# Kernel optimization log

Measured on AMD Instinct MI355X. Metric: run time of the kernel, lower is better.

The kernel has to match this reference:

```python
import jax, jax.numpy as jnp
import numpy as np

NEG_SLOPE = 0.2  # PyG GATConv default


def _gat_conv(x, src, dst, W, a_src, a_dst, b, heads, out_ch, concat, n):
    """PyG-style GATConv. src/dst already include self-loops. a_*: (heads, out_ch)."""
    h = (x @ W).reshape(n, heads, out_ch)                      # (n, H, C)
    alpha_s = jnp.einsum('nhc,hc->nh', h, a_src)               # (n, H)
    alpha_d = jnp.einsum('nhc,hc->nh', h, a_dst)
    e = jax.nn.leaky_relu(alpha_s[src] + alpha_d[dst], NEG_SLOPE)   # (Etot, H)
    # segment softmax over destination nodes (numerically stable)
    m = jax.ops.segment_max(e, dst, num_segments=n)            # (n, H)
    w = jnp.exp(e - m[dst])
    denom = jax.ops.segment_sum(w, dst, num_segments=n)
    att = w / (denom[dst] + 1e-16)                             # (Etot, H)
    out = jax.ops.segment_sum(h[src] * att[:, :, None], dst, num_segments=n)  # (n, H, C)
    out = out.reshape(n, heads * out_ch) if concat else out.mean(axis=1)
    return out + b


def setup_inputs() -> dict:
    key = jax.random.key(0)
    ks = jax.random.split(key, 16)
    N, E, D, Hc, H, M = 50000, 400000, 256, 128, 4, 256

    def glorot(k, shape):
        fan_in, fan_out = shape[0], int(np.prod(shape[1:]))
        std = float(np.sqrt(2.0 / (fan_in + fan_out)))
        return jax.random.normal(k, shape, dtype=jnp.float32) * std

    return {
        'x': jax.random.normal(ks[0], (N, D), dtype=jnp.float32),
        'edge_index': jax.random.randint(ks[1], (2, E), 0, N, dtype=jnp.int64),
        # encoder layer 1: D -> (H, Hc), concat
        'W1': glorot(ks[2], (D, H * Hc)),
        'a_src1': glorot(ks[3], (H, Hc)),
        'a_dst1': glorot(ks[4], (H, Hc)),
        'b1': jnp.zeros((H * Hc,), dtype=jnp.float32),
        'prelu_a': jnp.full((1,), 0.25, dtype=jnp.float32),
        # encoder layer 2: H*Hc -> M, 1 head, no concat
        'W2': glorot(ks[5], (H * Hc, M)),
        'a_src2': glorot(ks[6], (1, M)),
        'a_dst2': glorot(ks[7], (1, M)),
        'b2': jnp.zeros((M,), dtype=jnp.float32),
        # decoder: M -> D, 1 head, no concat
        'Wd': glorot(ks[8], (M, D)),
        'a_srcd': glorot(ks[9], (1, D)),
        'a_dstd': glorot(ks[10], (1, D)),
        'bd': jnp.zeros((D,), dtype=jnp.float32),
    }


def reference(x, edge_index, W1, a_src1, a_dst1, b1, prelu_a,
              W2, a_src2, a_dst2, b2, Wd, a_srcd, a_dstd, bd):
    n = x.shape[0]
    loop = jnp.arange(n, dtype=edge_index.dtype)
    src = jnp.concatenate([edge_index[0], loop])  # self-loops (PyG default)
    dst = jnp.concatenate([edge_index[1], loop])

    # --- encoder (eval mode: no masking, dropout off) ---
    h = _gat_conv(x, src, dst, W1, a_src1, a_dst1, b1, heads=4, out_ch=128, concat=True, n=n)
    h = jnp.where(h >= 0, h, prelu_a * h)  # PReLU
    z = _gat_conv(h, src, dst, W2, a_src2, a_dst2, b2, heads=1, out_ch=256, concat=False, n=n)

    # --- decoder (single GAT, no activation) ---
    x_hat = _gat_conv(z, src, dst, Wd, a_srcd, a_dstd, bd, heads=1, out_ch=256, concat=False, n=n)
    return (z, x_hat)
```

## Files before the change

### kernel.cpp

```cpp
#include <hip/hip_runtime.h>
#include <hip/hip_bf16.h>
#include <cstdint>

#define NEG_SLOPE 0.2f

typedef _Float16 f16x8 __attribute__((ext_vector_type(8)));
typedef float f32x4 __attribute__((ext_vector_type(4)));

union H2 { uint32_t u; _Float16 f[2]; };
union H4 { uint2 u2; _Float16 f[4]; };

__global__ void k_init_counts(int* __restrict__ counts, int n) {
  int i = blockIdx.x * blockDim.x + threadIdx.x;
  if (i < n) counts[i] = 1;
}

__global__ void k_hist(const int* __restrict__ dst, int* __restrict__ counts, int e) {
  int i = blockIdx.x * blockDim.x + threadIdx.x;
  if (i < e) atomicAdd(&counts[dst[i]], 1);
}

__global__ void k_scan1(const int* __restrict__ counts, int* __restrict__ pref,
                        int* __restrict__ bsum, int n) {
  __shared__ int sh[256];
  int tid = threadIdx.x;
  int i = blockIdx.x * 256 + tid;
  int v = (i < n) ? counts[i] : 0;
  sh[tid] = v;
  __syncthreads();
  for (int off = 1; off < 256; off <<= 1) {
    int t = (tid >= off) ? sh[tid - off] : 0;
    __syncthreads();
    sh[tid] += t;
    __syncthreads();
  }
  if (i < n) pref[i] = sh[tid];
  if (tid == 255) bsum[blockIdx.x] = sh[255];
}

__global__ void k_scan2(int* __restrict__ bsum, int nb) {
  __shared__ int sh[256];
  int tid = threadIdx.x;
  int v = (tid < nb) ? bsum[tid] : 0;
  sh[tid] = v;
  __syncthreads();
  for (int off = 1; off < 256; off <<= 1) {
    int t = (tid >= off) ? sh[tid - off] : 0;
    __syncthreads();
    sh[tid] += t;
    __syncthreads();
  }
  if (tid < nb) bsum[tid] = sh[tid];
}

__global__ void k_scan3(const int* __restrict__ pref, const int* __restrict__ bsum,
                        int* __restrict__ rowptr, int n) {
  int i = blockIdx.x * blockDim.x + threadIdx.x;
  if (i < n) rowptr[i + 1] = pref[i] + (blockIdx.x ? bsum[blockIdx.x - 1] : 0);
  if (i == 0) rowptr[0] = 0;
}

__global__ void k_init_csr(const int* __restrict__ rowptr, int* __restrict__ cursor,
                           int* __restrict__ csr_src, int n) {
  int i = blockIdx.x * blockDim.x + threadIdx.x;
  if (i < n) { int r = rowptr[i]; csr_src[r] = i; cursor[i] = r + 1; }
}

__global__ void k_fill(const int* __restrict__ src, const int* __restrict__ dst,
                       int* __restrict__ cursor, int* __restrict__ csr_src, int e) {
  int i = blockIdx.x * blockDim.x + threadIdx.x;
  if (i < e) { int p = atomicAdd(&cursor[dst[i]], 1); csr_src[p] = src[i]; }
}

__global__ void k_w2h(const float* __restrict__ W, _Float16* __restrict__ Wt, int K, int N) {
  int i = blockIdx.x * blockDim.x + threadIdx.x;
  if (i < K * N) {
    int k = i / N, n = i - k * N;
    Wt[(size_t)n * K + k] = (_Float16)W[i];
  }
}

template <bool A_F32>
__global__ __launch_bounds__(512) void k_gemm_f16(
    const void* __restrict__ Av, const _Float16* __restrict__ Bt,
    _Float16* __restrict__ C, int M, int N, int K) {
  __shared__ _Float16 As[256 * 72];
  __shared__ _Float16 Bs[128 * 72];
  const int tid  = threadIdx.x;
  const int lane = tid & 63;
  const int wid  = tid >> 6;
  const int wm = wid >> 1;
  const int wn = wid & 1;
  const int row0 = blockIdx.y * 256, col0 = blockIdx.x * 128;
  const int l15 = lane & 15, l16 = lane >> 4;
  const int srow = tid >> 3;
  const int skc  = (tid & 7) * 8;

  f32x4 acc[4][4] = {};

  for (int k0 = 0; k0 < K; k0 += 64) {
#pragma unroll
    for (int p = 0; p < 4; ++p) {
      int r = p * 64 + srow;
      int gr = row0 + r; if (gr > M - 1) gr = M - 1;
      _Float16 tmp[8];
      if constexpr (A_F32) {
        const float* src = (const float*)Av + (size_t)gr * K + k0 + skc;
        float4 v0 = ((const float4*)src)[0];
        float4 v1 = ((const float4*)src)[1];
        tmp[0] = (_Float16)v0.x; tmp[1] = (_Float16)v0.y;
        tmp[2] = (_Float16)v0.z; tmp[3] = (_Float16)v0.w;
        tmp[4] = (_Float16)v1.x; tmp[5] = (_Float16)v1.y;
        tmp[6] = (_Float16)v1.z; tmp[7] = (_Float16)v1.w;
      } else {
        const _Float16* src = (const _Float16*)Av + (size_t)gr * K + k0 + skc;
        *(uint4*)tmp = *(const uint4*)src;
      }
      *(uint4*)&As[r * 72 + skc] = *(uint4*)tmp;
    }
#pragma unroll
    for (int p = 0; p < 2; ++p) {
      int nr_ = p * 64 + srow;
      const _Float16* src = Bt + (size_t)(col0 + nr_) * K + k0 + skc;
      *(uint4*)&Bs[nr_ * 72 + skc] = *(const uint4*)src;
    }
    __syncthreads();
#pragma unroll
    for (int ks = 0; ks < 2; ++ks) {
      f16x8 bfrag[4];
#pragma unroll
      for (int nr = 0; nr < 4; ++nr)
        bfrag[nr] = *(const f16x8*)&Bs[(wn * 64 + nr * 16 + l15) * 72 + ks * 32 + l16 * 8];
#pragma unroll
      for (int mr = 0; mr < 4; ++mr) {
        f16x8 afrag = *(const f16x8*)&As[(wm * 64 + mr * 16 + l15) * 72 + ks * 32 + l16 * 8];
#pragma unroll
        for (int nr = 0; nr < 4; ++nr)
          acc[mr][nr] = __builtin_amdgcn_mfma_f32_16x16x32_f16(afrag, bfrag[nr], acc[mr][nr], 0, 0, 0);
      }
    }
    __syncthreads();
  }
#pragma unroll
  for (int mr = 0; mr < 4; ++mr) {
#pragma unroll
    for (int j = 0; j < 4; ++j) {
      int rg = row0 + wm * 64 + mr * 16 + l16 * 4 + j;
      if (rg < M) {
#pragma unroll
        for (int nr = 0; nr < 4; ++nr) {
          int cg = col0 + wn * 64 + nr * 16 + l15;
          C[(size_t)rg * N + cg] = (_Float16)acc[mr][nr][j];
        }
      }
    }
  }
}

template <int H, int CH>
__global__ void k_alpha(const _Float16* __restrict__ h, const float* __restrict__ a_src,
                        const float* __restrict__ a_dst, float* __restrict__ as,
                        float* __restrict__ ad, int total) {
  int wid = (blockIdx.x * blockDim.x + threadIdx.x) >> 6;
  int lane = threadIdx.x & 63;
  if (wid >= total) return;
  int head = wid % H;
  const _Float16* hp = h + (size_t)wid * CH;
  const float* asp = a_src + head * CH;
  const float* adp = a_dst + head * CH;
  float s1 = 0.f, s2 = 0.f;
  for (int c = lane * 2; c < CH; c += 128) {
    H2 v; v.u = *(const uint32_t*)&hp[c];
    float v0 = (float)v.f[0], v1 = (float)v.f[1];
    s1 += v0 * asp[c] + v1 * asp[c + 1];
    s2 += v0 * adp[c] + v1 * adp[c + 1];
  }
#pragma unroll
  for (int off = 32; off; off >>= 1) {
    s1 += __shfl_down(s1, off);
    s2 += __shfl_down(s2, off);
  }
  if (lane == 0) { as[wid] = s1; ad[wid] = s2; }
}

template <int W>
__device__ __forceinline__ float grp_sum(float v) {
#pragma unroll
  for (int o = W / 2; o; o >>= 1) v += __shfl_xor(v, o);
  return v;
}

template <int CT, int H, int ACT, int WF, int WH, int NPB>
__global__ __launch_bounds__(256) void k_agg(
    const _Float16* __restrict__ h, const float* __restrict__ as,
    const float* __restrict__ ad, const int* __restrict__ rowptr,
    const int* __restrict__ csr, const float* __restrict__ bias,
    const float* __restrict__ prelu_a, float* __restrict__ outf,
    _Float16* __restrict__ outh, int n) {
  constexpr int CH  = CT / H;
  constexpr int TPN = CT / 4;
  constexpr int HPW = (TPN >= 64) ? (64 / (CH / 4)) : 1;
  constexpr int EC  = 64 / HPW;

  int t = threadIdx.x;
  int node = blockIdx.x * NPB + t / TPN;
  if (node >= n) return;
  int nt = t % TPN;
  int c0 = nt * 4;
  int head = c0 / CH;
  int lane = t & 63;
  int grp = (EC == 64) ? 0 : (lane >> 5);
  int gl = lane & (EC - 1);
  int srcbase = grp * EC;

  int beg = rowptr[node];
  int cnt = rowptr[node + 1] - beg;
  float adv = ad[node * H + head];

  float denom = 0.f;
  float a0 = 0.f, a1 = 0.f, a2 = 0.f, a3 = 0.f;
  for (int b = 0; b < cnt; b += EC) {
    int i = b + gl;
    float w = 0.f; int s = 0;
    if (i < cnt) {
      s = csr[beg + i];
      float v = as[s * H + head] + adv;
      v = (v >= 0.f) ? v : NEG_SLOPE * v;
      w = __expf(v);
    }
    denom += grp_sum<EC>(w);
    int nedge = cnt - b; if (nedge > EC) nedge = EC;
    int kk = 0;
    for (; kk + 8 <= nedge; kk += 8) {
      int sj[8]; float wj[8]; H4 uj[8];
#pragma unroll
      for (int j = 0; j < 8; ++j) {
        sj[j] = __shfl(s, srcbase + kk + j);
        wj[j] = __shfl(w, srcbase + kk + j);
      }
#pragma unroll
      for (int j = 0; j < 8; ++j)
        uj[j].u2 = *(const uint2*)&h[(size_t)sj[j] * CT + c0];
#pragma unroll
      for (int j = 0; j < 8; ++j) {
        a0 += wj[j] * (float)uj[j].f[0];
        a1 += wj[j] * (float)uj[j].f[1];
        a2 += wj[j] * (float)uj[j].f[2];
        a3 += wj[j] * (float)uj[j].f[3];
      }
    }
    {
      int rem = nedge - kk;
      int sj[7]; float wj[7]; H4 uj[7];
#pragma unroll
      for (int j = 0; j < 7; ++j) {
        if (j < rem) {
          sj[j] = __shfl(s, srcbase + kk + j);
          wj[j] = __shfl(w, srcbase + kk + j);
        }
      }
#pragma unroll
      for (int j = 0; j < 7; ++j)
        if (j < rem) uj[j].u2 = *(const uint2*)&h[(size_t)sj[j] * CT + c0];
#pragma unroll
      for (int j = 0; j < 7; ++j) {
        if (j < rem) {
          a0 += wj[j] * (float)uj[j].f[0];
          a1 += wj[j] * (float)uj[j].f[1];
          a2 += wj[j] * (float)uj[j].f[2];
          a3 += wj[j] * (float)uj[j].f[3];
        }
      }
    }
  }

  float inv = 1.f / (denom + 1e-16f);
  float4 bv = *(const float4*)&bias[c0];
  float o0 = a0 * inv + bv.x;
  float o1 = a1 * inv + bv.y;
  float o2 = a2 * inv + bv.z;
  float o3 = a3 * inv + bv.w;
  if (ACT) {
    float a = prelu_a[0];
    o0 = (o0 >= 0.f) ? o0 : a * o0;
    o1 = (o1 >= 0.f) ? o1 : a * o1;
    o2 = (o2 >= 0.f) ? o2 : a * o2;
    o3 = (o3 >= 0.f) ? o3 : a * o3;
  }
  if (WF) {
    float4 o = make_float4(o0, o1, o2, o3);
    *(float4*)&outf[(size_t)node * CT + c0] = o;
  }
  if (WH) {
    H4 p;
    p.f[0] = (_Float16)o0; p.f[1] = (_Float16)o1;
    p.f[2] = (_Float16)o2; p.f[3] = (_Float16)o3;
    *(uint2*)&outh[(size_t)node * CT + c0] = p.u2;
  }
}

extern "C" void kernel_launch(void* const* d_in, const int* in_sizes, int n_in,
                              void* d_out, int out_size, void* d_ws, size_t ws_size,
                              hipStream_t stream) {
  const float* x      = (const float*)d_in[0];
  const int*   ei     = (const int*)d_in[1];
  const float* W1     = (const float*)d_in[2];
  const float* a_s1   = (const float*)d_in[3];
  const float* a_d1   = (const float*)d_in[4];
  const float* b1     = (const float*)d_in[5];
  const float* prelu  = (const float*)d_in[6];
  const float* W2     = (const float*)d_in[7];
  const float* a_s2   = (const float*)d_in[8];
  const float* a_d2   = (const float*)d_in[9];
  const float* b2     = (const float*)d_in[10];
  const float* Wd     = (const float*)d_in[11];
  const float* a_sd   = (const float*)d_in[12];
  const float* a_dd   = (const float*)d_in[13];
  const float* bd     = (const float*)d_in[14];

  const int N = in_sizes[0] / 256;
  const int E = in_sizes[1] / 2;
  const int* e_src = ei;
  const int* e_dst = ei + E;

  float* z    = (float*)d_out;
  float* xhat = z + (size_t)N * 256;

  _Float16* out1_h = (_Float16*)xhat;

  char* wp = (char*)d_ws;
  auto alloc = [&](size_t bytes) { char* p = wp; wp += (bytes + 15) & ~(size_t)15; return p; };
  _Float16* h_h  = (_Float16*)alloc((size_t)N * 512 * 2);
  float* alpS    = (float*)alloc((size_t)N * 4 * 4);
  float* alpD    = (float*)alloc((size_t)N * 4 * 4);
  int* rowptr    = (int*)alloc((size_t)(N + 1) * 4);
  int* csr       = (int*)alloc((size_t)(E + N) * 4);
  int* cursor    = (int*)alloc((size_t)N * 4);
  int* counts    = (int*)alloc((size_t)N * 4);
  int* pref      = (int*)alloc((size_t)N * 4);
  int* bsum      = (int*)alloc((size_t)256 * 4);
  _Float16* Wt1  = (_Float16*)alloc((size_t)512 * 256 * 2);
  _Float16* Wt2  = (_Float16*)alloc((size_t)256 * 512 * 2);
  _Float16* Wtd  = (_Float16*)alloc((size_t)256 * 256 * 2);

  const int B = 256;
  const int gN = (N + B - 1) / B;
  const int gE = (E + B - 1) / B;

  k_init_counts<<<gN, B, 0, stream>>>(counts, N);
  k_hist<<<gE, B, 0, stream>>>(e_dst, counts, E);
  k_scan1<<<gN, B, 0, stream>>>(counts, pref, bsum, N);
  k_scan2<<<1, B, 0, stream>>>(bsum, gN);
  k_scan3<<<gN, B, 0, stream>>>(pref, bsum, rowptr, N);
  k_init_csr<<<gN, B, 0, stream>>>(rowptr, cursor, csr, N);
  k_fill<<<gE, B, 0, stream>>>(e_src, e_dst, cursor, csr, E);

  k_w2h<<<(256 * 512 + B - 1) / B, B, 0, stream>>>(W1, Wt1, 256, 512);
  k_w2h<<<(512 * 256 + B - 1) / B, B, 0, stream>>>(W2, Wt2, 512, 256);
  k_w2h<<<(256 * 256 + B - 1) / B, B, 0, stream>>>(Wd, Wtd, 256, 256);

  const int gy = (N + 255) / 256;

  {
    dim3 grid(512 / 128, gy);
    k_gemm_f16<true><<<grid, 512, 0, stream>>>(x, Wt1, h_h, N, 512, 256);
    int tot = N * 4;
    k_alpha<4, 128><<<(tot * 64 + B - 1) / B, B, 0, stream>>>(h_h, a_s1, a_d1, alpS, alpD, tot);
    k_agg<512, 4, 1, 0, 1, 2><<<(N + 1) / 2, B, 0, stream>>>(
        h_h, alpS, alpD, rowptr, csr, b1, prelu, nullptr, out1_h, N);
  }

  {
    dim3 grid(256 / 128, gy);
    k_gemm_f16<false><<<grid, 512, 0, stream>>>(out1_h, Wt2, h_h, N, 256, 512);
    k_alpha<1, 256><<<(N * 64 + B - 1) / B, B, 0, stream>>>(h_h, a_s2, a_d2, alpS, alpD, N);
    k_agg<256, 1, 0, 1, 0, 4><<<(N + 3) / 4, B, 0, stream>>>(
        h_h, alpS, alpD, rowptr, csr, b2, prelu, z, nullptr, N);
  }

  {
    dim3 grid(256 / 128, gy);
    k_gemm_f16<true><<<grid, 512, 0, stream>>>(z, Wtd, h_h, N, 256, 256);
    k_alpha<1, 256><<<(N * 64 + B - 1) / B, B, 0, stream>>>(h_h, a_sd, a_dd, alpS, alpD, N);
    k_agg<256, 1, 0, 1, 0, 4><<<(N + 3) / 4, B, 0, stream>>>(
        h_h, alpS, alpD, rowptr, csr, bd, prelu, xhat, nullptr, N);
  }
}
```

Baseline: 591.0 us.

## Widen aggregation loads to 8 halves and use grid-stride persistent node loop

The GAT aggregation kernel now has each thread own 8 fp16 channels with 16-byte loads instead of 4 channels with 8-byte loads. Edge chunks are sized to match the per-head lane group. A fixed grid of 2048 blocks loops over nodes in grid-stride fashion instead of launching one block per few nodes. The aim is fewer, wider memory transactions and less block launch overhead. The cost is more registers per thread, smaller edge batches per shuffle round, and possible load imbalance from the fixed grid.

```diff
diff --git a/kernel.cpp b/kernel.cpp
--- a/kernel.cpp
+++ b/kernel.cpp
@@ -8,7 +8,7 @@
 typedef float f32x4 __attribute__((ext_vector_type(4)));
 
 union H2 { uint32_t u; _Float16 f[2]; };
-union H4 { uint2 u2; _Float16 f[4]; };
+union H8 { uint4 u4; _Float16 f[8]; };
 
 __global__ void k_init_counts(int* __restrict__ counts, int n) {
   int i = blockIdx.x * blockDim.x + threadIdx.x;
@@ -190,7 +190,7 @@
   return v;
 }
 
-template <int CT, int H, int ACT, int WF, int WH, int NPB>
+template <int CT, int H, int ACT, int WF, int WH>
 __global__ __launch_bounds__(256) void k_agg(
     const _Float16* __restrict__ h, const float* __restrict__ as,
     const float* __restrict__ ad, const int* __restrict__ rowptr,
@@ -198,104 +198,101 @@
     const float* __restrict__ prelu_a, float* __restrict__ outf,
     _Float16* __restrict__ outh, int n) {
   constexpr int CH  = CT / H;
-  constexpr int TPN = CT / 4;
-  constexpr int HPW = (TPN >= 64) ? (64 / (CH / 4)) : 1;
-  constexpr int EC  = 64 / HPW;
-
-  int t = threadIdx.x;
-  int node = blockIdx.x * NPB + t / TPN;
-  if (node >= n) return;
-  int nt = t % TPN;
-  int c0 = nt * 4;
+  constexpr int TPN = CT / 8;
+  constexpr int NSW = 64 / TPN;
+  constexpr int G   = CH / 8;
+
+  int lane = threadIdx.x & 63;
+  int wib  = threadIdx.x >> 6;
+  int slot0  = (blockIdx.x * (256 >> 6) + wib) * NSW + ((NSW == 2) ? (lane >> 5) : 0);
+  int stride = gridDim.x * (256 >> 6) * NSW;
+  int nt   = lane & (TPN - 1);
+  int c0   = nt * 8;
   int head = c0 / CH;
-  int lane = t & 63;
-  int grp = (EC == 64) ? 0 : (lane >> 5);
-  int gl = lane & (EC - 1);
-  int srcbase = grp * EC;
-
-  int beg = rowptr[node];
-  int cnt = rowptr[node + 1] - beg;
-  float adv = ad[node * H + head];
-
-  float denom = 0.f;
-  float a0 = 0.f, a1 = 0.f, a2 = 0.f, a3 = 0.f;
-  for (int b = 0; b < cnt; b += EC) {
-    int i = b + gl;
-    float w = 0.f; int s = 0;
-    if (i < cnt) {
-      s = csr[beg + i];
-      float v = as[s * H + head] + adv;
-      v = (v >= 0.f) ? v : NEG_SLOPE * v;
-      w = __expf(v);
-    }
-    denom += grp_sum<EC>(w);
-    int nedge = cnt - b; if (nedge > EC) nedge = EC;
-    int kk = 0;
-    for (; kk + 8 <= nedge; kk += 8) {
-      int sj[8]; float wj[8]; H4 uj[8];
-#pragma unroll
-      for (int j = 0; j < 8; ++j) {
-        sj[j] = __shfl(s, srcbase + kk + j);
-        wj[j] = __shfl(w, srcbase + kk + j);
-      }
-#pragma unroll
-      for (int j = 0; j < 8; ++j)
-        uj[j].u2 = *(const uint2*)&h[(size_t)sj[j] * CT + c0];
-#pragma unroll
-      for (int j = 0; j < 8; ++j) {
-        a0 += wj[j] * (float)uj[j].f[0];
-        a1 += wj[j] * (float)uj[j].f[1];
-        a2 += wj[j] * (float)uj[j].f[2];
-        a3 += wj[j] * (float)uj[j].f[3];
-      }
-    }
-    {
-      int rem = nedge - kk;
-      int sj[7]; float wj[7]; H4 uj[7];
-#pragma unroll
-      for (int j = 0; j < 7; ++j) {
-        if (j < rem) {
+  int gl   = lane & (G - 1);
+  int srcbase = (lane / G) * G;
+
+  float a_prelu = ACT ? prelu_a[0] : 0.f;
+  float4 bv0 = *(const float4*)&bias[c0];
+  float4 bv1 = *(const float4*)&bias[c0 + 4];
+
+  for (int node = slot0; node < n; node += stride) {
+    int beg = rowptr[node];
+    int cnt = rowptr[node + 1] - beg;
+    float adv = ad[node * H + head];
+    float denom = 0.f;
+    float acc[8] = {};
+    for (int b = 0; b < cnt; b += G) {
+      int i = b + gl;
+      float w = 0.f; int s = 0;
+      if (i < cnt) {
+        s = csr[beg + i];
+        float v = as[s * H + head] + adv;
+        v = (v >= 0.f) ? v : NEG_SLOPE * v;
+        w = __expf(v);
+      }
+      denom += grp_sum<G>(w);
+      int nedge = cnt - b; if (nedge > G) nedge = G;
+      int kk = 0;
+      for (; kk + 4 <= nedge; kk += 4) {
+        int sj[4]; float wj[4]; H8 uj[4];
+#pragma unroll
+        for (int j = 0; j < 4; ++j) {
           sj[j] = __shfl(s, srcbase + kk + j);
           wj[j] = __shfl(w, srcbase + kk + j);
         }
-      }
-#pragma unroll
-      for (int j = 0; j < 7; ++j)
-        if (j < rem) uj[j].u2 = *(const uint2*)&h[(size_t)sj[j] * CT + c0];
-#pragma unroll
-      for (int j = 0; j < 7; ++j) {
-        if (j < rem) {
-          a0 += wj[j] * (float)uj[j].f[0];
-          a1 += wj[j] * (float)uj[j].f[1];
-          a2 += wj[j] * (float)uj[j].f[2];
-          a3 += wj[j] * (float)uj[j].f[3];
-        }
-      }
-    }
-  }
-
-  float inv = 1.f / (denom + 1e-16f);
-  float4 bv = *(const float4*)&bias[c0];
-  float o0 = a0 * inv + bv.x;
-  float o1 = a1 * inv + bv.y;
-  float o2 = a2 * inv + bv.z;
-  float o3 = a3 * inv + bv.w;
-  if (ACT) {
-    float a = prelu_a[0];
-    o0 = (o0 >= 0.f) ? o0 : a * o0;
-    o1 = (o1 >= 0.f) ? o1 : a * o1;
-    o2 = (o2 >= 0.f) ? o2 : a * o2;
-    o3 = (o3 >= 0.f) ? o3 : a * o3;
-  }
-  if (WF) {
-    float4 o = make_float4(o0, o1, o2, o3);
-    *(float4*)&outf[(size_t)node * CT + c0] = o;
-  }
-  if (WH) {
-    H4 p;
-    p.f[0] = (_Float16)o0; p.f[1] = (_Float16)o1;
-    p.f[2] = (_Float16)o2; p.f[3] = (_Float16)o3;
-    *(uint2*)&outh[(size_t)node * CT + c0] = p.u2;
+#pragma unroll
+        for (int j = 0; j < 4; ++j)
+          uj[j].u4 = *(const uint4*)&h[(size_t)sj[j] * CT + c0];
+#pragma unroll
+        for (int j = 0; j < 4; ++j) {
+#pragma unroll
+          for (int q = 0; q < 8; ++q) acc[q] += wj[j] * (float)uj[j].f[q];
+        }
+      }
+      {
+        int rem = nedge - kk;
+        int sj[3]; float wj[3]; H8 uj[3];
+#pragma unroll
+        for (int j = 0; j < 3; ++j) {
+          if (j < rem) {
+            sj[j] = __shfl(s, srcbase + kk + j);
+            wj[j] = __shfl(w, srcbase + kk + j);
+          }
+        }
+#pragma unroll
+        for (int j = 0; j < 3; ++j)
+          if (j < rem) uj[j].u4 = *(const uint4*)&h[(size_t)sj[j] * CT + c0];
+#pragma unroll
+        for (int j = 0; j < 3; ++j) {
+          if (j < rem) {
+#pragma unroll
+            for (int q = 0; q < 8; ++q) acc[q] += wj[j] * (float)uj[j].f[q];
+          }
+        }
+      }
+    }
+
+    float inv = 1.f / (denom + 1e-16f);
+    float o[8];
+    o[0] = acc[0] * inv + bv0.x; o[1] = acc[1] * inv + bv0.y;
+    o[2] = acc[2] * inv + bv0.z; o[3] = acc[3] * inv + bv0.w;
+    o[4] = acc[4] * inv + bv1.x; o[5] = acc[5] * inv + bv1.y;
+    o[6] = acc[6] * inv + bv1.z; o[7] = acc[7] * inv + bv1.w;
+    if (ACT) {
+#pragma unroll
+      for (int q = 0; q < 8; ++q) o[q] = (o[q] >= 0.f) ? o[q] : a_prelu * o[q];
+    }
+    if (WF) {
+      *(float4*)&outf[(size_t)node * CT + c0]     = make_float4(o[0], o[1], o[2], o[3]);
+      *(float4*)&outf[(size_t)node * CT + c0 + 4] = make_float4(o[4], o[5], o[6], o[7]);
+    }
+    if (WH) {
+      H8 p;
+#pragma unroll
+      for (int q = 0; q < 8; ++q) p.f[q] = (_Float16)o[q];
+      *(uint4*)&outh[(size_t)node * CT + c0] = p.u4;
+    }
   }
 }
 
@@ -346,6 +343,7 @@
   const int B = 256;
   const int gN = (N + B - 1) / B;
   const int gE = (E + B - 1) / B;
+  const int AGG_GRID = 2048;
 
   k_init_counts<<<gN, B, 0, stream>>>(counts, N);
   k_hist<<<gE, B, 0, stream>>>(e_dst, counts, E);
@@ -366,7 +364,7 @@
     k_gemm_f16<true><<<grid, 512, 0, stream>>>(x, Wt1, h_h, N, 512, 256);
     int tot = N * 4;
     k_alpha<4, 128><<<(tot * 64 + B - 1) / B, B, 0, stream>>>(h_h, a_s1, a_d1, alpS, alpD, tot);
-    k_agg<512, 4, 1, 0, 1, 2><<<(N + 1) / 2, B, 0, stream>>>(
+    k_agg<512, 4, 1, 0, 1><<<AGG_GRID, B, 0, stream>>>(
         h_h, alpS, alpD, rowptr, csr, b1, prelu, nullptr, out1_h, N);
   }
 
@@ -374,7 +372,7 @@
     dim3 grid(256 / 128, gy);
     k_gemm_f16<false><<<grid, 512, 0, stream>>>(out1_h, Wt2, h_h, N, 256, 512);
     k_alpha<1, 256><<<(N * 64 + B - 1) / B, B, 0, stream>>>(h_h, a_s2, a_d2, alpS, alpD, N);
-    k_agg<256, 1, 0, 1, 0, 4><<<(N + 3) / 4, B, 0, stream>>>(
+    k_agg<256, 1, 0, 1, 0><<<AGG_GRID, B, 0, stream>>>(
         h_h, alpS, alpD, rowptr, csr, b2, prelu, z, nullptr, N);
   }
 
@@ -382,7 +380,7 @@
     dim3 grid(256 / 128, gy);
     k_gemm_f16<true><<<grid, 512, 0, stream>>>(z, Wtd, h_h, N, 256, 256);
     k_alpha<1, 256><<<(N * 64 + B - 1) / B, B, 0, stream>>>(h_h, a_sd, a_dd, alpS, alpD, N);
-    k_agg<256, 1, 0, 1, 0, 4><<<(N + 3) / 4, B, 0, stream>>>(
+    k_agg<256, 1, 0, 1, 0><<<AGG_GRID, B, 0, stream>>>(
         h_h, alpS, alpD, rowptr, csr, bd, prelu, xhat, nullptr, N);
   }
 }
```

Result: faster. 524.9 us (-11.2%).
